# Kernel tuning notes

Hardware: AMD Instinct MI355X
Metric: run time of the kernel (lower is better)

The kernel has to match this reference:

```python
import jax, jax.numpy as jnp
import numpy as np

DIM = 512
HEADS = 8
DIM_HEAD = 64
INNER = HEADS * DIM_HEAD  # 512
BN_EPS = 1e-5


def _bn(x, gamma, beta, mean, var):
    # BatchNorm1d in eval mode over channel axis 1 of [b, c, n]
    inv = gamma / jnp.sqrt(var + BN_EPS)
    return x * inv[None, :, None] + (beta - mean * inv)[None, :, None]


def setup_inputs() -> dict:
    key = jax.random.key(0)
    ks = jax.random.split(key, 12)
    b, d, n = 4, DIM, 2048
    s = 0.02
    return {
        "x": jax.random.normal(ks[0], (b, d, n), dtype=jnp.float32),
        "W_qkv": jax.random.normal(ks[1], (3 * INNER, DIM), dtype=jnp.float32) * s,
        "W_out": jax.random.normal(ks[2], (DIM, INNER), dtype=jnp.float32) * s,
        "b_out": jax.random.normal(ks[3], (DIM,), dtype=jnp.float32) * s,
        "g1": jax.random.normal(ks[4], (DIM,), dtype=jnp.float32) * 0.1 + 1.0,
        "beta1": jax.random.normal(ks[5], (DIM,), dtype=jnp.float32) * 0.1,
        "m1": jax.random.normal(ks[6], (DIM,), dtype=jnp.float32) * 0.1,
        "v1": jax.random.uniform(ks[7], (DIM,), minval=0.5, maxval=1.5, dtype=jnp.float32),
        "W_ffn": jax.random.normal(ks[8], (DIM, DIM), dtype=jnp.float32) * s,
        "g2": jax.random.normal(ks[9], (DIM,), dtype=jnp.float32) * 0.1 + 1.0,
        "beta2": jax.random.normal(ks[10], (DIM,), dtype=jnp.float32) * 0.1,
        "m2": jax.random.normal(ks[11], (DIM,), dtype=jnp.float32) * 0.1,
        "v2": jax.random.uniform(jax.random.fold_in(key, 99), (DIM,), minval=0.5, maxval=1.5, dtype=jnp.float32),
    }


def reference(x, W_qkv, W_out, b_out, g1, beta1, m1, v1, W_ffn, g2, beta2, m2, v2):
    b, d, n = x.shape
    h, dh = HEADS, DIM_HEAD
    scale = dh ** -0.5

    # ---- Attention (manual QKV + einsum softmax attention) ----
    xt = jnp.einsum("bdn->bnd", x)                       # [b, n, d]
    qkv = xt @ W_qkv.T                                   # [b, n, 3*inner]
    q, k, v = jnp.split(qkv, 3, axis=-1)
    def to_heads(t):
        return t.reshape(b, n, h, dh).transpose(0, 2, 1, 3)  # [b, h, n, dh]
    q, k, v = to_heads(q), to_heads(k), to_heads(v)
    dots = jnp.einsum("bhid,bhjd->bhij", q, k) * scale   # [b, h, n, n]
    attn = jax.nn.softmax(dots, axis=-1)
    out = jnp.einsum("bhij,bhjd->bhid", attn, v)         # [b, h, n, dh]
    out = out.transpose(0, 2, 1, 3).reshape(b, n, h * dh).transpose(0, 2, 1)  # [b, inner, n]
    # to_out: Conv1d(inner, dim, 1, bias=True) + BatchNorm1d(dim)
    out = jnp.einsum("oc,bcn->bon", W_out, out) + b_out[None, :, None]
    att_out = _bn(out, g1, beta1, m1, v1)

    # ---- Residual + GELU, then FFN (Conv1d 1x1 no bias + BN), residual + GELU ----
    att = jax.nn.gelu(att_out + x, approximate=False)
    ffn = _bn(jnp.einsum("oc,bcn->bon", W_ffn, att), g2, beta2, m2, v2)
    return jax.nn.gelu(att + ffn, approximate=False)
```

## Files before the change

kernel.cpp:

```cpp
#include <hip/hip_runtime.h>
#include <math.h>

#define N_TOK 2048

typedef __attribute__((ext_vector_type(8))) short short8;
typedef __attribute__((ext_vector_type(4))) float f32x4;
typedef __attribute__((ext_vector_type(16))) float f32x16;

__device__ __forceinline__ float gelu_f(float v) {
    return 0.5f * v * (1.0f + erff(v * 0.7071067811865475f));
}
__device__ __forceinline__ ushort f2bf(float x) {
    uint u = __float_as_uint(x);
    uint r = u + 0x7FFFu + ((u >> 16) & 1u);
    return (ushort)(r >> 16);
}
__device__ __forceinline__ float bf2f(ushort u) {
    return __uint_as_float((uint)u << 16);
}
__device__ __forceinline__ void gload16(const void* g, void* s) {
    __builtin_amdgcn_global_load_lds((const __attribute__((address_space(1))) void*)g,
                                     (__attribute__((address_space(3))) void*)s, 16, 0, 0);
}

__global__ __launch_bounds__(256)
void prep(const float* __restrict__ w0, ushort* __restrict__ o0,
          const float* __restrict__ w1, ushort* __restrict__ o1,
          const float* __restrict__ w2, ushort* __restrict__ o2,
          const float* __restrict__ x, ushort* __restrict__ xt)
{
    __shared__ ushort sT[64 * 68];
    const int tid = threadIdx.x;
    int bx = blockIdx.x;
    if (bx < 1280) {
        int i4 = bx * 256 + tid;
        const float* src; ushort* dst; int idx;
        if (i4 < 196608)      { src = w0; dst = o0; idx = i4; }
        else if (i4 < 262144) { src = w1; dst = o1; idx = i4 - 196608; }
        else                  { src = w2; dst = o2; idx = i4 - 262144; }
        float4 v = *(const float4*)&src[idx * 4];
        ushort4 p; p.x = f2bf(v.x); p.y = f2bf(v.y); p.z = f2bf(v.z); p.w = f2bf(v.w);
        *(ushort4*)&dst[idx * 4] = p;
        return;
    }
    bx -= 1280;
    const int tok0 = (bx & 31) * 64;
    const int ch0 = ((bx >> 5) & 7) * 64;
    const int bi = bx >> 8;
    #pragma unroll
    for (int i = 0; i < 4; i++) {
        int ch = (tid >> 4) + i * 16;
        int t4 = (tid & 15) * 4;
        float4 v = *(const float4*)&x[((size_t)bi * 512 + ch0 + ch) * N_TOK + tok0 + t4];
        ushort4 p; p.x = f2bf(v.x); p.y = f2bf(v.y); p.z = f2bf(v.z); p.w = f2bf(v.w);
        *(ushort4*)&sT[ch * 68 + t4] = p;
    }
    __syncthreads();
    const int tr = (tid & 15) + (tid >> 6) * 16;
    const int cb = ((tid >> 4) & 3) * 16;
    uint vv[8];
    #pragma unroll
    for (int j = 0; j < 8; j++) {
        uint lo = sT[(cb + 2 * j) * 68 + tr];
        uint hi = sT[(cb + 2 * j + 1) * 68 + tr];
        vv[j] = lo | (hi << 16);
    }
    size_t base = ((size_t)bi * N_TOK + tok0 + tr) * 512 + ch0 + cb;
    *(uint4*)&xt[base]     = *(uint4*)&vv[0];
    *(uint4*)&xt[base + 8] = *(uint4*)&vv[4];
}

template<int MODE, int BM, int BN>
__global__ __launch_bounds__(256)
void bgemm(const ushort* __restrict__ A, const ushort* __restrict__ Bt, int M,
           ushort* __restrict__ qt, ushort* __restrict__ vc,
           float* __restrict__ outF, ushort* __restrict__ outB,
           const float* __restrict__ bias,
           const float* __restrict__ g, const float* __restrict__ be,
           const float* __restrict__ mu, const float* __restrict__ va,
           const ushort* __restrict__ residB)
{
    constexpr int MF = BM / 32, NF = BN / 32;
    __shared__ ushort sA[2][BM * 64];
    __shared__ ushort sB[2][BN * 64];
    const int tid = threadIdx.x;
    const int w = tid >> 6, l = tid & 63;
    const int l16 = l & 15, lg = l >> 4;
    const int wr = w >> 1, wc = w & 1;
    const int bi = blockIdx.z;
    const int m0 = blockIdx.y * BM, n0 = blockIdx.x * BN;
    const ushort* Bb = Bt + (size_t)bi * N_TOK * 512;
    const int srow = l >> 3, spos = l & 7;

    f32x4 acc[MF][NF];
    #pragma unroll
    for (int i = 0; i < MF; i++)
        #pragma unroll
        for (int j = 0; j < NF; j++) acc[i][j] = (f32x4){0.f, 0.f, 0.f, 0.f};

#define GSTAGE(T, BUF) \
    { \
        const int kt_ = (T) * 64; \
        _Pragma("unroll") \
        for (int i_ = 0; i_ < BM / 32; i_++) { \
            int row_ = w * (BM / 4) + i_ * 8 + srow; \
            int c_ = spos ^ (row_ & 7); \
            gload16(A + (size_t)(m0 + row_) * 512 + kt_ + c_ * 8, \
                    &sA[BUF][(w * (BM / 4) + i_ * 8) * 64]); \
        } \
        _Pragma("unroll") \
        for (int i_ = 0; i_ < BN / 32; i_++) { \
            int row_ = w * (BN / 4) + i_ * 8 + srow; \
            int c_ = spos ^ (row_ & 7); \
            gload16(Bb + (size_t)(n0 + row_) * 512 + kt_ + c_ * 8, \
                    &sB[BUF][(w * (BN / 4) + i_ * 8) * 64]); \
        } \
    }

    GSTAGE(0, 0)

    for (int t = 0; t < 8; t++) {
        asm volatile("s_waitcnt vmcnt(0)" ::: "memory");
        __builtin_amdgcn_s_barrier();
        __builtin_amdgcn_sched_barrier(0);
        if (t + 1 < 8) { GSTAGE(t + 1, (t + 1) & 1) }
        const int cur = t & 1;

        #pragma unroll
        for (int ks = 0; ks < 2; ks++) {
            short8 af[MF], bfv[NF];
            #pragma unroll
            for (int mi = 0; mi < MF; mi++) {
                int row = wr * (BM / 2) + mi * 16 + l16;
                af[mi] = *(const short8*)&sA[cur][row * 64 +
                          (((ks * 4 + lg) ^ (row & 7)) << 3)];
            }
            #pragma unroll
            for (int ni = 0; ni < NF; ni++) {
                int row = wc * (BN / 2) + ni * 16 + l16;
                bfv[ni] = *(const short8*)&sB[cur][row * 64 +
                           (((ks * 4 + lg) ^ (row & 7)) << 3)];
            }
            __builtin_amdgcn_s_setprio(1);
            #pragma unroll
            for (int mi = 0; mi < MF; mi++)
                #pragma unroll
                for (int ni = 0; ni < NF; ni++)
                    acc[mi][ni] = __builtin_amdgcn_mfma_f32_16x16x32_bf16(
                        af[mi], bfv[ni], acc[mi][ni], 0, 0, 0);
            __builtin_amdgcn_s_setprio(0);
        }
    }
#undef GSTAGE

    const int chb = m0 + wr * (BM / 2);
    const int tkb = n0 + wc * (BN / 2);
    if (MODE == 0) {
        if (m0 < 1024) {
            const float qs = (m0 < 512) ? 0.18033688f : 1.0f;
            #pragma unroll
            for (int mi = 0; mi < MF; mi++) {
                int ob = chb + mi * 16 + lg * 4;
                #pragma unroll
                for (int ni = 0; ni < NF; ni++) {
                    int tok = tkb + ni * 16 + l16;
                    ushort4 p;
                    p.x = f2bf(acc[mi][ni][0] * qs); p.y = f2bf(acc[mi][ni][1] * qs);
                    p.z = f2bf(acc[mi][ni][2] * qs); p.w = f2bf(acc[mi][ni][3] * qs);
                    *(ushort4*)&qt[((size_t)bi * N_TOK + tok) * 1024 + ob] = p;
                }
            }
        } else {
            #pragma unroll
            for (int mi = 0; mi < MF; mi++)
                #pragma unroll
                for (int r = 0; r < 4; r++) {
                    int o = chb + mi * 16 + lg * 4 + r - 1024;
                    #pragma unroll
                    for (int ni = 0; ni < NF; ni++) {
                        int tok = tkb + ni * 16 + l16;
                        vc[((size_t)bi * 512 + o) * N_TOK + tok] = f2bf(acc[mi][ni][r]);
                    }
                }
        }
    } else {
        #pragma unroll
        for (int mi = 0; mi < MF; mi++) {
            float inv[4], sh[4], bb[4];
            #pragma unroll
            for (int r = 0; r < 4; r++) {
                int o = chb + mi * 16 + lg * 4 + r;
                inv[r] = g[o] * rsqrtf(va[o] + 1e-5f);
                sh[r]  = be[o] - mu[o] * inv[r];
                bb[r]  = (MODE == 1) ? bias[o] : 0.f;
            }
            #pragma unroll
            for (int ni = 0; ni < NF; ni++) {
                int tok = tkb + ni * 16 + l16;
                ushort4 rv = *(const ushort4*)&residB[((size_t)bi * N_TOK + tok) * 512 +
                                                      chb + mi * 16 + lg * 4];
                float rr_[4] = {bf2f(rv.x), bf2f(rv.y), bf2f(rv.z), bf2f(rv.w)};
                float ov[4];
                #pragma unroll
                for (int r = 0; r < 4; r++) {
                    float y = (acc[mi][ni][r] + bb[r]) * inv[r] + sh[r];
                    ov[r] = gelu_f((MODE == 1) ? (y + rr_[r]) : (rr_[r] + y));
                }
                if (MODE == 1) {
                    ushort4 p;
                    p.x = f2bf(ov[0]); p.y = f2bf(ov[1]);
                    p.z = f2bf(ov[2]); p.w = f2bf(ov[3]);
                    *(ushort4*)&outB[((size_t)bi * N_TOK + tok) * 512 +
                                     chb + mi * 16 + lg * 4] = p;
                } else {
                    #pragma unroll
                    for (int r = 0; r < 4; r++) {
                        int o = chb + mi * 16 + lg * 4 + r;
                        outF[((size_t)bi * 512 + o) * N_TOK + tok] = ov[r];
                    }
                }
            }
        }
    }
}

__global__ __launch_bounds__(512)
void attn_mfma(const ushort* __restrict__ qt, const ushort* __restrict__ vc,
               ushort* __restrict__ aout)
{
    __shared__ ushort sK[3][64 * 64];
    __shared__ ushort sV[3][64 * 64];
    const int tid = threadIdx.x;
    const int w = tid >> 6, l = tid & 63;
    const int c = l & 31, h = l >> 5;
    const int phys = blockIdx.x;
    const int logi = (phys & 7) * 32 + (phys >> 3);
    const int qblk = logi & 7;
    const int pair = logi >> 3;
    const int hh = pair & 7, bi = pair >> 3;
    const int qw = qblk * 256 + w * 32;
    const int srow = l >> 3, spos = l & 7;

    const ushort* kSrc = qt + (size_t)bi * N_TOK * 1024 + 512 + hh * 64 + ((spos ^ srow) << 3);
    const ushort* vSrc = vc + (size_t)(bi * 512 + hh * 64) * N_TOK + ((spos ^ srow) << 3);

    short8 qf[4];
    #pragma unroll
    for (int dk = 0; dk < 4; dk++)
        qf[dk] = *(const short8*)(qt +
            (size_t)(bi * N_TOK + qw + c) * 1024 + hh * 64 + dk * 16 + h * 8);

    f32x16 oacc[2];
    #pragma unroll
    for (int dt = 0; dt < 2; dt++)
        #pragma unroll
        for (int i = 0; i < 16; i++) oacc[dt][i] = 0.f;
    float lsum = 0.f;

#define STAGE(T, BUF) \
    { \
        const int kv0_ = (T) * 64; \
        const int rb_ = w * 8; \
        gload16(kSrc + (size_t)(kv0_ + rb_ + srow) * 1024, &sK[BUF][rb_ * 64]); \
        gload16(vSrc + (size_t)(rb_ + srow) * N_TOK + kv0_, &sV[BUF][rb_ * 64]); \
    }

    STAGE(0, 0)
    STAGE(1, 1)

    const int NT = N_TOK / 64;
    for (int t = 0; t < NT; t++) {
        if (t < NT - 1) { asm volatile("s_waitcnt vmcnt(2)" ::: "memory"); }
        else            { asm volatile("s_waitcnt vmcnt(0)" ::: "memory"); }
        __builtin_amdgcn_s_barrier();
        __builtin_amdgcn_sched_barrier(0);
        const int b_c = t % 3;
        if (t + 2 < NT) { STAGE(t + 2, (t + 2) % 3) }

        const ushort* kB = &sK[b_c][0];
        const ushort* vB = &sV[b_c][0];

        #pragma unroll
        for (int s = 0; s < 2; s++) {
            f32x16 sacc;
            #pragma unroll
            for (int i = 0; i < 16; i++) sacc[i] = 0.f;
            __builtin_amdgcn_s_setprio(1);
            #pragma unroll
            for (int dk = 0; dk < 4; dk++) {
                int row = s * 32 + c;
                short8 kf = *(const short8*)&kB[row * 64 +
                             (((dk * 2 + h) ^ (row & 7)) << 3)];
                sacc = __builtin_amdgcn_mfma_f32_32x32x16_bf16(kf, qf[dk], sacc, 0, 0, 0);
            }
            __builtin_amdgcn_s_setprio(0);

            uint u0_0, u0_1, u1_0, u1_1, u2_0, u2_1, u3_0, u3_1;
            float ps = 0.f;
            {
                float p0, p1, p2, p3;
#define PACK_G(G, U0, U1) \
                p0 = __builtin_amdgcn_exp2f(sacc[4*G+0]); \
                p1 = __builtin_amdgcn_exp2f(sacc[4*G+1]); \
                p2 = __builtin_amdgcn_exp2f(sacc[4*G+2]); \
                p3 = __builtin_amdgcn_exp2f(sacc[4*G+3]); \
                ps += (p0 + p1) + (p2 + p3); \
                asm("v_cvt_pk_bf16_f32 %0, %1, %2" : "=v"(U0) : "v"(p0), "v"(p1)); \
                asm("v_cvt_pk_bf16_f32 %0, %1, %2" : "=v"(U1) : "v"(p2), "v"(p3));
                PACK_G(0, u0_0, u0_1)
                PACK_G(1, u1_0, u1_1)
                PACK_G(2, u2_0, u2_1)
                PACK_G(3, u3_0, u3_1)
#undef PACK_G
            }
            lsum += ps;

#define PV_STEP(T2, A0, A1, B0, B1) \
            { \
                uint a0 = A0, b0 = B0, a1 = A1, b1 = B1; \
                asm volatile("v_permlane32_swap_b32 %0, %1" : "+v"(b0), "+v"(a0)); \
                asm volatile("v_permlane32_swap_b32 %0, %1" : "+v"(b1), "+v"(a1)); \
                uint4 fu = make_uint4(a0, a1, b0, b1); \
                short8 pf = *(short8*)&fu; \
                __builtin_amdgcn_s_setprio(1); \
                _Pragma("unroll") \
                for (int dt = 0; dt < 2; dt++) { \
                    int row = dt * 32 + c; \
                    short8 vf = *(const short8*)&vB[row * 64 + \
                                 (((s * 4 + T2 * 2 + h) ^ (row & 7)) << 3)]; \
                    oacc[dt] = __builtin_amdgcn_mfma_f32_32x32x16_bf16( \
                        pf, vf, oacc[dt], 0, 0, 0); \
                } \
                __builtin_amdgcn_s_setprio(0); \
            }
            PV_STEP(0, u0_0, u0_1, u1_0, u1_1)
            PV_STEP(1, u2_0, u2_1, u3_0, u3_1)
#undef PV_STEP
        }
    }
#undef STAGE

    lsum += __shfl_xor(lsum, 32);
    float rl = 1.f / lsum;
    #pragma unroll
    for (int dt = 0; dt < 2; dt++)
        #pragma unroll
        for (int g = 0; g < 4; g++) {
            float o0 = oacc[dt][4 * g + 0] * rl;
            float o1 = oacc[dt][4 * g + 1] * rl;
            float o2 = oacc[dt][4 * g + 2] * rl;
            float o3 = oacc[dt][4 * g + 3] * rl;
            uint p0, p1;
            asm("v_cvt_pk_bf16_f32 %0, %1, %2" : "=v"(p0) : "v"(o0), "v"(o1));
            asm("v_cvt_pk_bf16_f32 %0, %1, %2" : "=v"(p1) : "v"(o2), "v"(o3));
            int ch = hh * 64 + dt * 32 + 8 * g + 4 * h;
            *(uint2*)&aout[((size_t)bi * N_TOK + qw + c) * 512 + ch] = make_uint2(p0, p1);
        }
}

extern "C" void kernel_launch(void* const* d_in, const int* in_sizes, int n_in,
                              void* d_out, int out_size, void* d_ws, size_t ws_size,
                              hipStream_t stream) {
    const float* x    = (const float*)d_in[0];
    const float* Wqkv = (const float*)d_in[1];
    const float* Wout = (const float*)d_in[2];
    const float* bout = (const float*)d_in[3];
    const float* g1   = (const float*)d_in[4];
    const float* be1  = (const float*)d_in[5];
    const float* m1   = (const float*)d_in[6];
    const float* v1   = (const float*)d_in[7];
    const float* Wffn = (const float*)d_in[8];
    const float* g2   = (const float*)d_in[9];
    const float* be2  = (const float*)d_in[10];
    const float* m2   = (const float*)d_in[11];
    const float* v2   = (const float*)d_in[12];

    char* ws = (char*)d_ws;
    ushort* wqB  = (ushort*)(ws + 0);
    ushort* woB  = (ushort*)(ws + 1572864);
    ushort* wfB  = (ushort*)(ws + 2097152);
    ushort* xt   = (ushort*)(ws + 2621440);
    ushort* qtp  = (ushort*)(ws + 11010048);
    ushort* vcp  = (ushort*)(ws + 27787264);
    ushort* aout = (ushort*)(ws + 36175872);
    ushort* attB = (ushort*)(ws + 27787264);

    dim3 blk(256);
    prep<<<2304, blk, 0, stream>>>(Wqkv, wqB, Wout, woB, Wffn, wfB, x, xt);
    bgemm<0, 128, 128><<<dim3(16, 12, 4), blk, 0, stream>>>(
        wqB, xt, 1536, qtp, vcp, nullptr, nullptr,
        nullptr, nullptr, nullptr, nullptr, nullptr, nullptr);
    attn_mfma<<<dim3(256), dim3(512), 0, stream>>>(qtp, vcp, aout);
    bgemm<1, 64, 128><<<dim3(16, 8, 4), blk, 0, stream>>>(
        woB, aout, 512, nullptr, nullptr, nullptr, attB,
        bout, g1, be1, m1, v1, xt);
    bgemm<2, 64, 128><<<dim3(16, 8, 4), blk, 0, stream>>>(
        wfB, attB, 512, nullptr, nullptr, (float*)d_out, nullptr,
        nullptr, g2, be2, m2, v2, attB);
}
```

Baseline: 111.1 us.

## Load K/V fragments directly into registers, bypassing LDS staging

The attention kernel drops its triple-buffered LDS staging of K and V tiles, along with the per-tile barrier. Each wave now loads its MFMA K and V operand fragments straight from global memory into registers, double-buffered across two tiles. This removes the LDS traffic and workgroup synchronisation. In exchange, each of the 8 waves loads the same K/V data separately (8x the global/L2 traffic), and the register pressure from 32 short8 buffers may lower occupancy or cause spills.

```diff
diff --git a/kernel.cpp b/kernel.cpp
--- a/kernel.cpp
+++ b/kernel.cpp
@@ -224,12 +224,66 @@
     }
 }
 
+__device__ __forceinline__ void tile_compute(const short8* kf, const short8* vf,
+                                             const short8* qf, f32x16* oacc,
+                                             float& lsum)
+{
+    #pragma unroll
+    for (int s = 0; s < 2; s++) {
+        f32x16 sacc;
+        #pragma unroll
+        for (int i = 0; i < 16; i++) sacc[i] = 0.f;
+        __builtin_amdgcn_s_setprio(1);
+        #pragma unroll
+        for (int dk = 0; dk < 4; dk++)
+            sacc = __builtin_amdgcn_mfma_f32_32x32x16_bf16(kf[s * 4 + dk], qf[dk],
+                                                           sacc, 0, 0, 0);
+        __builtin_amdgcn_s_setprio(0);
+
+        uint u0_0, u0_1, u1_0, u1_1, u2_0, u2_1, u3_0, u3_1;
+        float ps = 0.f;
+        {
+            float p0, p1, p2, p3;
+#define PACK_G(G, U0, U1) \
+            p0 = __builtin_amdgcn_exp2f(sacc[4*G+0]); \
+            p1 = __builtin_amdgcn_exp2f(sacc[4*G+1]); \
+            p2 = __builtin_amdgcn_exp2f(sacc[4*G+2]); \
+            p3 = __builtin_amdgcn_exp2f(sacc[4*G+3]); \
+            ps += (p0 + p1) + (p2 + p3); \
+            asm("v_cvt_pk_bf16_f32 %0, %1, %2" : "=v"(U0) : "v"(p0), "v"(p1)); \
+            asm("v_cvt_pk_bf16_f32 %0, %1, %2" : "=v"(U1) : "v"(p2), "v"(p3));
+            PACK_G(0, u0_0, u0_1)
+            PACK_G(1, u1_0, u1_1)
+            PACK_G(2, u2_0, u2_1)
+            PACK_G(3, u3_0, u3_1)
+#undef PACK_G
+        }
+        lsum += ps;
+
+#define PV_STEP(T2, A0, A1, B0, B1) \
+        { \
+            uint a0 = A0, b0 = B0, a1 = A1, b1 = B1; \
+            asm volatile("v_permlane32_swap_b32 %0, %1" : "+v"(b0), "+v"(a0)); \
+            asm volatile("v_permlane32_swap_b32 %0, %1" : "+v"(b1), "+v"(a1)); \
+            uint4 fu = make_uint4(a0, a1, b0, b1); \
+            short8 pf = *(short8*)&fu; \
+            __builtin_amdgcn_s_setprio(1); \
+            _Pragma("unroll") \
+            for (int dt = 0; dt < 2; dt++) \
+                oacc[dt] = __builtin_amdgcn_mfma_f32_32x32x16_bf16( \
+                    pf, vf[(s * 2 + T2) * 2 + dt], oacc[dt], 0, 0, 0); \
+            __builtin_amdgcn_s_setprio(0); \
+        }
+        PV_STEP(0, u0_0, u0_1, u1_0, u1_1)
+        PV_STEP(1, u2_0, u2_1, u3_0, u3_1)
+#undef PV_STEP
+    }
+}
+
 __global__ __launch_bounds__(512)
 void attn_mfma(const ushort* __restrict__ qt, const ushort* __restrict__ vc,
                ushort* __restrict__ aout)
 {
-    __shared__ ushort sK[3][64 * 64];
-    __shared__ ushort sV[3][64 * 64];
     const int tid = threadIdx.x;
     const int w = tid >> 6, l = tid & 63;
     const int c = l & 31, h = l >> 5;
@@ -239,10 +293,10 @@
     const int pair = logi >> 3;
     const int hh = pair & 7, bi = pair >> 3;
     const int qw = qblk * 256 + w * 32;
-    const int srow = l >> 3, spos = l & 7;
-
-    const ushort* kSrc = qt + (size_t)bi * N_TOK * 1024 + 512 + hh * 64 + ((spos ^ srow) << 3);
-    const ushort* vSrc = vc + (size_t)(bi * 512 + hh * 64) * N_TOK + ((spos ^ srow) << 3);
+
+    const ushort* Kl = qt + (size_t)bi * N_TOK * 1024 + 512 + hh * 64
+                          + (size_t)c * 1024 + h * 8;
+    const ushort* Vl = vc + (size_t)(bi * 512 + hh * 64 + c) * N_TOK + h * 8;
 
     short8 qf[4];
     #pragma unroll
@@ -257,88 +311,33 @@
         for (int i = 0; i < 16; i++) oacc[dt][i] = 0.f;
     float lsum = 0.f;
 
-#define STAGE(T, BUF) \
+#define LOADKV(KD, VD, T) \
     { \
-        const int kv0_ = (T) * 64; \
-        const int rb_ = w * 8; \
-        gload16(kSrc + (size_t)(kv0_ + rb_ + srow) * 1024, &sK[BUF][rb_ * 64]); \
-        gload16(vSrc + (size_t)(rb_ + srow) * N_TOK + kv0_, &sV[BUF][rb_ * 64]); \
-    }
-
-    STAGE(0, 0)
-    STAGE(1, 1)
-
-    const int NT = N_TOK / 64;
-    for (int t = 0; t < NT; t++) {
-        if (t < NT - 1) { asm volatile("s_waitcnt vmcnt(2)" ::: "memory"); }
-        else            { asm volatile("s_waitcnt vmcnt(0)" ::: "memory"); }
-        __builtin_amdgcn_s_barrier();
-        __builtin_amdgcn_sched_barrier(0);
-        const int b_c = t % 3;
-        if (t + 2 < NT) { STAGE(t + 2, (t + 2) % 3) }
-
-        const ushort* kB = &sK[b_c][0];
-        const ushort* vB = &sV[b_c][0];
-
-        #pragma unroll
-        for (int s = 0; s < 2; s++) {
-            f32x16 sacc;
-            #pragma unroll
-            for (int i = 0; i < 16; i++) sacc[i] = 0.f;
-            __builtin_amdgcn_s_setprio(1);
-            #pragma unroll
-            for (int dk = 0; dk < 4; dk++) {
-                int row = s * 32 + c;
-                short8 kf = *(const short8*)&kB[row * 64 +
-                             (((dk * 2 + h) ^ (row & 7)) << 3)];
-                sacc = __builtin_amdgcn_mfma_f32_32x32x16_bf16(kf, qf[dk], sacc, 0, 0, 0);
-            }
-            __builtin_amdgcn_s_setprio(0);
-
-            uint u0_0, u0_1, u1_0, u1_1, u2_0, u2_1, u3_0, u3_1;
-            float ps = 0.f;
-            {
-                float p0, p1, p2, p3;
-#define PACK_G(G, U0, U1) \
-                p0 = __builtin_amdgcn_exp2f(sacc[4*G+0]); \
-                p1 = __builtin_amdgcn_exp2f(sacc[4*G+1]); \
-                p2 = __builtin_amdgcn_exp2f(sacc[4*G+2]); \
-                p3 = __builtin_amdgcn_exp2f(sacc[4*G+3]); \
-                ps += (p0 + p1) + (p2 + p3); \
-                asm("v_cvt_pk_bf16_f32 %0, %1, %2" : "=v"(U0) : "v"(p0), "v"(p1)); \
-                asm("v_cvt_pk_bf16_f32 %0, %1, %2" : "=v"(U1) : "v"(p2), "v"(p3));
-                PACK_G(0, u0_0, u0_1)
-                PACK_G(1, u1_0, u1_1)
-                PACK_G(2, u2_0, u2_1)
-                PACK_G(3, u3_0, u3_1)
-#undef PACK_G
-            }
-            lsum += ps;
-
-#define PV_STEP(T2, A0, A1, B0, B1) \
-            { \
-                uint a0 = A0, b0 = B0, a1 = A1, b1 = B1; \
-                asm volatile("v_permlane32_swap_b32 %0, %1" : "+v"(b0), "+v"(a0)); \
-                asm volatile("v_permlane32_swap_b32 %0, %1" : "+v"(b1), "+v"(a1)); \
-                uint4 fu = make_uint4(a0, a1, b0, b1); \
-                short8 pf = *(short8*)&fu; \
-                __builtin_amdgcn_s_setprio(1); \
-                _Pragma("unroll") \
-                for (int dt = 0; dt < 2; dt++) { \
-                    int row = dt * 32 + c; \
-                    short8 vf = *(const short8*)&vB[row * 64 + \
-                                 (((s * 4 + T2 * 2 + h) ^ (row & 7)) << 3)]; \
-                    oacc[dt] = __builtin_amdgcn_mfma_f32_32x32x16_bf16( \
-                        pf, vf, oacc[dt], 0, 0, 0); \
-                } \
-                __builtin_amdgcn_s_setprio(0); \
-            }
-            PV_STEP(0, u0_0, u0_1, u1_0, u1_1)
-            PV_STEP(1, u2_0, u2_1, u3_0, u3_1)
-#undef PV_STEP
-        }
-    }
-#undef STAGE
+        const ushort* kp_ = Kl + (size_t)(T) * 64 * 1024; \
+        _Pragma("unroll") \
+        for (int s_ = 0; s_ < 2; s_++) \
+            _Pragma("unroll") \
+            for (int dk_ = 0; dk_ < 4; dk_++) \
+                KD[s_ * 4 + dk_] = *(const short8*)(kp_ + (size_t)s_ * 32 * 1024 + dk_ * 16); \
+        const ushort* vp_ = Vl + (T) * 64; \
+        _Pragma("unroll") \
+        for (int s2_ = 0; s2_ < 4; s2_++) \
+            _Pragma("unroll") \
+            for (int dt_ = 0; dt_ < 2; dt_++) \
+                VD[s2_ * 2 + dt_] = *(const short8*)(vp_ + (size_t)dt_ * 32 * N_TOK + s2_ * 16); \
+    }
+
+    short8 kA[8], vA[8], kB[8], vB8[8];
+    LOADKV(kA, vA, 0)
+    LOADKV(kB, vB8, 1)
+
+    for (int t = 0; t < 32; t += 2) {
+        tile_compute(kA, vA, qf, oacc, lsum);
+        if (t + 2 < 32) { LOADKV(kA, vA, t + 2) }
+        tile_compute(kB, vB8, qf, oacc, lsum);
+        if (t + 3 < 32) { LOADKV(kB, vB8, t + 3) }
+    }
+#undef LOADKV
 
     lsum += __shfl_xor(lsum, 32);
     float rl = 1.f / lsum;
```

Measured after the change: 191.6 us. +72.4%, slower.
